# Kernel tuning notes

Measured on AMD Instinct MI355X. Metric: run time of the kernel, lower is better.

Reference implementation:

```python
import jax, jax.numpy as jnp
import numpy as np

LORA_SCALING = 1.0 / 4.0  # lora_alpha / lora_rank
NUM_HEADS = 16
HEAD_DIM = 64
ROPE_BASE = 20000.0


def rotate_half(x):
    x1, x2 = jnp.split(x, 2, axis=-1)
    return jnp.concatenate([-x2, x1], axis=-1)


def setup_inputs() -> dict:
    key = jax.random.key(0)
    ks = jax.random.split(key, 8)
    B, S, D = 8, 1024, 1024
    hidden_states = jax.random.normal(ks[0], (B, S, D), jnp.float32)
    attention_mask = jnp.zeros((B, 1, 1, S), jnp.float32)
    # real rotary tables (HF style: duplicated half-dim freqs)
    inv_freq = 1.0 / (ROPE_BASE ** (jnp.arange(0, HEAD_DIM, 2, dtype=jnp.float32) / HEAD_DIM))
    t = jnp.arange(S, dtype=jnp.float32)
    freqs = jnp.outer(t, inv_freq)                      # [S, hd/2]
    emb = jnp.concatenate([freqs, freqs], axis=-1)      # [S, hd]
    cos = jnp.broadcast_to(jnp.cos(emb)[None], (B, S, HEAD_DIM))
    sin = jnp.broadcast_to(jnp.sin(emb)[None], (B, S, HEAD_DIM))
    adapter_mask = jax.random.randint(ks[1], (B,), 0, 5, jnp.int32)
    Wqkv_weight = jax.random.normal(ks[2], (3 * D, D), jnp.float32) * 0.02
    Wqkv_bias = jax.random.normal(ks[3], (3 * D,), jnp.float32) * 0.02
    lora_A = jax.random.normal(ks[4], (5, 4, D), jnp.float32) * 0.02
    lora_B = jax.random.normal(ks[5], (5, 3 * D, 4), jnp.float32) * 0.02
    return dict(hidden_states=hidden_states, attention_mask=attention_mask,
                cos=cos, sin=sin, adapter_mask=adapter_mask,
                Wqkv_weight=Wqkv_weight, Wqkv_bias=Wqkv_bias,
                lora_A=lora_A, lora_B=lora_B)


def reference(hidden_states, attention_mask, cos, sin, adapter_mask,
              Wqkv_weight, Wqkv_bias, lora_A, lora_B):
    B, S, D = hidden_states.shape
    H, hd = NUM_HEADS, HEAD_DIM
    # fused QKV projection with per-task LoRA (gather adapters per batch row)
    base = jnp.einsum('bsd,od->bso', hidden_states, Wqkv_weight) + Wqkv_bias
    A_t = lora_A[adapter_mask]                    # [B, r, D]
    B_t = lora_B[adapter_mask]                    # [B, 3D, r]
    lo = jnp.einsum('bsd,brd->bsr', hidden_states, A_t)
    delta = jnp.einsum('bsr,bor->bso', lo, B_t) * LORA_SCALING
    qkv = (base + delta).reshape(B, S, 3, H, hd)
    q = qkv[:, :, 0].transpose(0, 2, 1, 3)        # [B,H,S,hd]
    k = qkv[:, :, 1].transpose(0, 2, 1, 3)
    v = qkv[:, :, 2].transpose(0, 2, 1, 3)
    # inline RoPE
    c = cos[:, None, :, :]
    s = sin[:, None, :, :]
    q = q * c + rotate_half(q) * s
    k = k * c + rotate_half(k) * s
    # eager SDPA
    scaling = hd ** -0.5
    scores = jnp.einsum('bhqd,bhkd->bhqk', q, k) * scaling + attention_mask
    attn = jax.nn.softmax(scores, axis=-1)
    out = jnp.einsum('bhqk,bhkd->bhqd', attn, v)
    return out.transpose(0, 2, 1, 3).reshape(B, S, H * hd)
```

## Files before the change

kernel.cpp:

```cpp
#include <hip/hip_runtime.h>
#include <hip/hip_bf16.h>
#include <stdint.h>

typedef __attribute__((ext_vector_type(8))) short short8;
typedef __attribute__((ext_vector_type(4))) float f32x4;
typedef unsigned short ushort_t;

#define MFMA16(a, b, c) __builtin_amdgcn_mfma_f32_16x16x32_bf16((a), (b), (c), 0, 0, 0)
#define EXP2F(x) __builtin_amdgcn_exp2f(x)
#define BAR() __builtin_amdgcn_s_barrier()
#define LGKM0() do { asm volatile("s_waitcnt lgkmcnt(0)" ::: "memory"); \
                     __builtin_amdgcn_sched_barrier(0); } while (0)


__device__ __forceinline__ float bf2f(unsigned short u) {
    union { unsigned int i; float f; } x; x.i = ((unsigned int)u) << 16; return x.f;
}
__device__ __forceinline__ unsigned short f2bf(float f) {
    union { float f; unsigned int i; } x; x.f = f;
    unsigned int i = x.i;
    i = i + 0x7FFFu + ((i >> 16) & 1u);
    return (unsigned short)(i >> 16);
}
__device__ __forceinline__ unsigned int pack2(float a, float b) {
    return (unsigned int)f2bf(a) | ((unsigned int)f2bf(b) << 16);
}
__device__ __forceinline__ void glds16(const void* gsrc, void* ldst) {
    __builtin_amdgcn_global_load_lds(
        (const __attribute__((address_space(1))) unsigned int*)gsrc,
        (__attribute__((address_space(3))) unsigned int*)ldst, 16, 0, 0);
}

__global__ __launch_bounds__(64) void prep_kernel(
    const float* __restrict__ hidden,
    const float* __restrict__ W,
    const float* __restrict__ loraA,
    const int* __restrict__ adapter_mask,
    ushort_t* __restrict__ Hb,
    ushort_t* __restrict__ Wb,
    float4* __restrict__ lo)
{
    int blk = blockIdx.x;
    int lane = threadIdx.x;
    if (blk < 8192) {
        int b = blk >> 10;
        int a = adapter_mask[b];
        const float* hp = hidden + (size_t)blk * 1024 + lane * 16;
        float hv[16];
        for (int j = 0; j < 16; ++j) hv[j] = hp[j];
        uint4 p0, p1;
        p0.x = pack2(hv[0], hv[1]);  p0.y = pack2(hv[2], hv[3]);
        p0.z = pack2(hv[4], hv[5]);  p0.w = pack2(hv[6], hv[7]);
        p1.x = pack2(hv[8], hv[9]);  p1.y = pack2(hv[10], hv[11]);
        p1.z = pack2(hv[12], hv[13]); p1.w = pack2(hv[14], hv[15]);
        uint4* hd = (uint4*)(Hb + (size_t)blk * 1024 + lane * 16);
        hd[0] = p0; hd[1] = p1;
        const float* Ap = loraA + (size_t)a * 4096 + lane * 16;
        float acc[4];
        for (int r = 0; r < 4; ++r) {
            const float* ap = Ap + r * 1024;
            float s = 0.f;
            for (int j = 0; j < 16; ++j) s += hv[j] * ap[j];
            acc[r] = s;
        }
        for (int off = 32; off > 0; off >>= 1)
            for (int r = 0; r < 4; ++r) acc[r] += __shfl_xor(acc[r], off);
        if (lane == 0) lo[blk] = make_float4(acc[0], acc[1], acc[2], acc[3]);
    } else {
        int row = blk - 8192;
        const float* wp = W + (size_t)row * 1024 + lane * 16;
        float wv[16];
        for (int j = 0; j < 16; ++j) wv[j] = wp[j];
        uint4 p0, p1;
        p0.x = pack2(wv[0], wv[1]);  p0.y = pack2(wv[2], wv[3]);
        p0.z = pack2(wv[4], wv[5]);  p0.w = pack2(wv[6], wv[7]);
        p1.x = pack2(wv[8], wv[9]);  p1.y = pack2(wv[10], wv[11]);
        p1.z = pack2(wv[12], wv[13]); p1.w = pack2(wv[14], wv[15]);
        uint4* wd = (uint4*)(Wb + (size_t)row * 1024 + lane * 16);
        wd[0] = p0; wd[1] = p1;
    }
}

__global__ __launch_bounds__(512, 2) void qkv_gemm_kernel(
    const ushort_t* __restrict__ Hb,
    const ushort_t* __restrict__ Wb,
    const float* __restrict__ bias,
    const float4* __restrict__ lo,
    const float* __restrict__ loraB,
    const int* __restrict__ adapter_mask,
    const float* __restrict__ cosp,
    const float* __restrict__ sinp,
    ushort_t* __restrict__ qw,
    ushort_t* __restrict__ kw,
    ushort_t* __restrict__ vt)
{
    __shared__ __align__(16) ushort_t As[2][16384];
    __shared__ __align__(16) ushort_t Bs[2][16384];
    int tid = threadIdx.x;
    int wave = tid >> 6, lane = tid & 63, quad = lane >> 4, l16 = lane & 15;
    int wm = wave >> 2, wn = wave & 3;

    int wg = (blockIdx.x & 7) * 48 + (blockIdx.x >> 3);
    int bx = wg % 12, by = wg / 12;
    int n0 = bx * 256;
    int m0 = by * 256;

    int r_ = tid >> 3, c_ = (tid & 7) ^ (r_ & 7);
    const ushort_t* pA0 = Hb + (size_t)(m0 +   0 + r_) * 1024 + c_ * 8;
    const ushort_t* pA1 = Hb + (size_t)(m0 +  64 + r_) * 1024 + c_ * 8;
    const ushort_t* pA2 = Hb + (size_t)(m0 + 128 + r_) * 1024 + c_ * 8;
    const ushort_t* pA3 = Hb + (size_t)(m0 + 192 + r_) * 1024 + c_ * 8;
    const ushort_t* pB0 = Wb + (size_t)(n0 +   0 + r_) * 1024 + c_ * 8;
    const ushort_t* pB1 = Wb + (size_t)(n0 +  64 + r_) * 1024 + c_ * 8;
    const ushort_t* pB2 = Wb + (size_t)(n0 + 128 + r_) * 1024 + c_ * 8;
    const ushort_t* pB3 = Wb + (size_t)(n0 + 192 + r_) * 1024 + c_ * 8;
    char* stA0 = (char*)&As[0][0] + wave * 1024;
    char* stB0 = (char*)&Bs[0][0] + wave * 1024;

    f32x4 acc[8][4];
#pragma unroll
    for (int i = 0; i < 8; ++i)
#pragma unroll
        for (int j = 0; j < 4; ++j) acc[i][j] = (f32x4)0.f;

    glds16(pB0, stB0);          glds16(pB1, stB0 + 8192);
    glds16(pB2, stB0 + 16384);  glds16(pB3, stB0 + 24576);
    glds16(pA0, stA0);          glds16(pA1, stA0 + 8192);
    glds16(pA2, stA0 + 16384);  glds16(pA3, stA0 + 24576);
    glds16(pB0 + 64, stB0 + 32768);          glds16(pB1 + 64, stB0 + 32768 + 8192);
    glds16(pB2 + 64, stB0 + 32768 + 16384);  glds16(pB3 + 64, stB0 + 32768 + 24576);

    short8 bfr[4][2];
    short8 af0[2], af1[2];

#define AREADS(p) do {                                                              \
        int rl0 = (p) * 32 + l16;                                                   \
        int rl1 = rl0 + 16;                                                         \
        int u0 = wm * 2 + (rl0 >> 6), u1 = wm * 2 + (rl1 >> 6);                     \
        int rr0 = rl0 & 63, rr1 = rl1 & 63;                                         \
        af0[0] = *(const short8*)(rdA + u0 * 8192 + (rr0 * 8 + ((quad    ) ^ (rr0 & 7))) * 16); \
        af0[1] = *(const short8*)(rdA + u0 * 8192 + (rr0 * 8 + ((quad + 4) ^ (rr0 & 7))) * 16); \
        af1[0] = *(const short8*)(rdA + u1 * 8192 + (rr1 * 8 + ((quad    ) ^ (rr1 & 7))) * 16); \
        af1[1] = *(const short8*)(rdA + u1 * 8192 + (rr1 * 8 + ((quad + 4) ^ (rr1 & 7))) * 16); \
    } while (0)

#define PMFMA(p) do {                                                    \
        __builtin_amdgcn_s_setprio(1);                                   \
        acc[2*(p)  ][0] = MFMA16(af0[0], bfr[0][0], acc[2*(p)  ][0]);    \
        acc[2*(p)  ][1] = MFMA16(af0[0], bfr[1][0], acc[2*(p)  ][1]);    \
        acc[2*(p)  ][2] = MFMA16(af0[0], bfr[2][0], acc[2*(p)  ][2]);    \
        acc[2*(p)  ][3] = MFMA16(af0[0], bfr[3][0], acc[2*(p)  ][3]);    \
        acc[2*(p)+1][0] = MFMA16(af1[0], bfr[0][0], acc[2*(p)+1][0]);    \
        acc[2*(p)+1][1] = MFMA16(af1[0], bfr[1][0], acc[2*(p)+1][1]);    \
        acc[2*(p)+1][2] = MFMA16(af1[0], bfr[2][0], acc[2*(p)+1][2]);    \
        acc[2*(p)+1][3] = MFMA16(af1[0], bfr[3][0], acc[2*(p)+1][3]);    \
        acc[2*(p)  ][0] = MFMA16(af0[1], bfr[0][1], acc[2*(p)  ][0]);    \
        acc[2*(p)  ][1] = MFMA16(af0[1], bfr[1][1], acc[2*(p)  ][1]);    \
        acc[2*(p)  ][2] = MFMA16(af0[1], bfr[2][1], acc[2*(p)  ][2]);    \
        acc[2*(p)  ][3] = MFMA16(af0[1], bfr[3][1], acc[2*(p)  ][3]);    \
        acc[2*(p)+1][0] = MFMA16(af1[1], bfr[0][1], acc[2*(p)+1][0]);    \
        acc[2*(p)+1][1] = MFMA16(af1[1], bfr[1][1], acc[2*(p)+1][1]);    \
        acc[2*(p)+1][2] = MFMA16(af1[1], bfr[2][1], acc[2*(p)+1][2]);    \
        acc[2*(p)+1][3] = MFMA16(af1[1], bfr[3][1], acc[2*(p)+1][3]);    \
        __builtin_amdgcn_s_setprio(0);                                   \
    } while (0)

#pragma unroll 2
    for (int t = 0; t < 16; ++t) {
        int cur = t & 1;
        const char* rdA = (const char*)&As[0][0] + cur * 32768;
        const char* rdB = (const char*)&Bs[0][0] + cur * 32768;
        char* sA = stA0 + (cur ^ 1) * 32768;
        char* sB = stB0 + cur * 32768;
        int kA = (t + 1) << 6;
        int kB = (t + 2) << 6;
        bool doA = (t < 15), doB = (t < 14);

        if (t < 15) { asm volatile("s_waitcnt vmcnt(4)" ::: "memory"); }
        else        { asm volatile("s_waitcnt vmcnt(0)" ::: "memory"); }
        BAR();
#pragma unroll
        for (int ni = 0; ni < 4; ++ni) {
            int rb = ni * 16 + l16;
            bfr[ni][0] = *(const short8*)(rdB + wn * 8192 + (rb * 8 + ((quad    ) ^ (rb & 7))) * 16);
            bfr[ni][1] = *(const short8*)(rdB + wn * 8192 + (rb * 8 + ((quad + 4) ^ (rb & 7))) * 16);
        }
        AREADS(0);
        if (doA) { glds16(pA0 + kA, sA); glds16(pA1 + kA, sA + 8192); }
        BAR();
        LGKM0();
        PMFMA(0);

        BAR();
        AREADS(1);
        if (doA) { glds16(pA2 + kA, sA + 16384); glds16(pA3 + kA, sA + 24576); }
        BAR();
        LGKM0();
        PMFMA(1);

        BAR();
        AREADS(2);
        if (doB) { glds16(pB0 + kB, sB); glds16(pB1 + kB, sB + 8192); }
        BAR();
        LGKM0();
        PMFMA(2);

        BAR();
        AREADS(3);
        if (doB) { glds16(pB2 + kB, sB + 16384); glds16(pB3 + kB, sB + 24576); }
        BAR();
        LGKM0();
        PMFMA(3);
    }
#undef AREADS
#undef PMFMA

    int t_qkv = n0 >> 10;
    int b = m0 >> 10;
    int a_idx = adapter_mask[b];
    float bi[4], bb[4][4];
    int cpos[4], chh[4];
#pragma unroll
    for (int ni = 0; ni < 4; ++ni) {
        int c = n0 + wn * 64 + ni * 16 + l16;
        bi[ni] = bias[c];
        const float* Bp = loraB + ((size_t)a_idx * 3072 + c) * 4;
        bb[ni][0] = Bp[0]; bb[ni][1] = Bp[1]; bb[ni][2] = Bp[2]; bb[ni][3] = Bp[3];
        cpos[ni] = c & 63; chh[ni] = (c >> 6) & 15;
    }
#pragma unroll
    for (int mi = 0; mi < 8; ++mi) {
        float vals[4][4];
        int mrow0 = m0 + wm * 128 + mi * 16 + quad * 4;
#pragma unroll
        for (int r = 0; r < 4; ++r) {
            float4 lov = lo[mrow0 + r];
#pragma unroll
            for (int ni = 0; ni < 4; ++ni)
                vals[r][ni] = acc[mi][ni][r] + bi[ni]
                      + 0.25f * (lov.x * bb[ni][0] + lov.y * bb[ni][1]
                               + lov.z * bb[ni][2] + lov.w * bb[ni][3]);
        }
        int s0 = mrow0 & 1023;
        if (t_qkv < 2) {
#pragma unroll
            for (int r = 0; r < 4; ++r) {
                int s = s0 + r;
                size_t cb = ((size_t)b * 1024 + s) * 64;
                float cA = cosp[cb + l16],      sA_ = sinp[cb + l16];
                float cB = cosp[cb + 16 + l16], sB_ = sinp[cb + 16 + l16];
                float w0 = vals[r][0] * cA - vals[r][2] * sA_;
                float w2 = vals[r][2] * cA + vals[r][0] * sA_;
                float w1 = vals[r][1] * cB - vals[r][3] * sB_;
                float w3 = vals[r][3] * cB + vals[r][1] * sB_;
                float v[4] = {w0, w1, w2, w3};
#pragma unroll
                for (int ni = 0; ni < 4; ++ni) {
                    size_t bh = (size_t)b * 16 + chh[ni];
                    ushort_t ob = f2bf(v[ni]);
                    if (t_qkv == 0) qw[(bh * 1024 + s) * 64 + cpos[ni]] = ob;
                    else            kw[(bh * 1024 + s) * 64 + cpos[ni]] = ob;
                }
            }
        } else {
#pragma unroll
            for (int ni = 0; ni < 4; ++ni) {
                uint2 pk;
                pk.x = pack2(vals[0][ni], vals[1][ni]);
                pk.y = pack2(vals[2][ni], vals[3][ni]);
                size_t bh = (size_t)b * 16 + chh[ni];
                *(uint2*)&vt[(bh * 64 + cpos[ni]) * 1024 + s0] = pk;
            }
        }
    }
}

__global__ __launch_bounds__(256) void attn_kernel(
    const ushort_t* __restrict__ qw,
    const ushort_t* __restrict__ kw,
    const ushort_t* __restrict__ vt,
    const float* __restrict__ mask,
    float* __restrict__ out)
{
    __shared__ __align__(16) ushort_t Kt[3][4096];
    __shared__ __align__(16) ushort_t Vt[3][4096];
    __shared__ __align__(16) ushort_t Ps[4][32][72];
    __shared__ float mlds[1024];
    const float KSCALE = 0.125f * 1.44269504f;
    int tid = threadIdx.x;
    int wave = tid >> 6, lane = tid & 63, quad = lane >> 4, l16 = lane & 15;
    int id = blockIdx.x;
    int qt = id >> 7;
    int bh = id & 127;
    int b = bh >> 4, h = bh & 15;
    size_t base = (size_t)bh * 65536;
    int q0 = qt * 128 + wave * 32;

    for (int i = tid; i < 1024; i += 256) mlds[i] = mask[b * 1024 + i] * 1.44269504f;

    const ushort_t* kbase = kw + base;
    const ushort_t* vbase = vt + base;

    int n0 = tid, n1 = tid + 256;
    int r0 = n0 >> 3, c0 = (n0 & 7) ^ (r0 & 7);
    int r1 = n1 >> 3, c1 = (n1 & 7) ^ (r1 & 7);

    short8 qf[2][2];
    for (int mt = 0; mt < 2; ++mt)
        for (int kt = 0; kt < 2; ++kt)
            qf[mt][kt] = *(const short8*)(qw + base + (size_t)(q0 + mt * 16 + l16) * 64 + kt * 32 + quad * 8);

    f32x4 oacc[2][4], sum_acc[2];
    for (int mt = 0; mt < 2; ++mt) {
        sum_acc[mt] = (f32x4)0.f;
        for (int nt = 0; nt < 4; ++nt) oacc[mt][nt] = (f32x4)0.f;
    }

    short8 ones;
    for (int j = 0; j < 8; ++j) ones[j] = (short)0x3F80;

    __syncthreads();

    int koff[4][2], voff[4][2];
    for (int nt = 0; nt < 4; ++nt)
        for (int kt = 0; kt < 2; ++kt) {
            int rr = nt * 16 + l16;
            int cc = (kt * 4 + quad) ^ (rr & 7);
            koff[nt][kt] = (rr * 8 + cc) * 8;
            voff[nt][kt] = (rr * 8 + cc) * 8;
        }

    {
        char* kd = (char*)&Kt[0][0] + wave * 1024;
        char* vd = (char*)&Vt[0][0] + wave * 1024;
        glds16(kbase + (size_t)r0 * 64 + c0 * 8, kd);
        glds16(kbase + (size_t)r1 * 64 + c1 * 8, kd + 4096);
        glds16(vbase + (size_t)r0 * 1024 + c0 * 8, vd);
        glds16(vbase + (size_t)r1 * 1024 + c1 * 8, vd + 4096);
        kd = (char*)&Kt[1][0] + wave * 1024;
        vd = (char*)&Vt[1][0] + wave * 1024;
        glds16(kbase + (size_t)(64 + r0) * 64 + c0 * 8, kd);
        glds16(kbase + (size_t)(64 + r1) * 64 + c1 * 8, kd + 4096);
        glds16(vbase + (size_t)r0 * 1024 + 64 + c0 * 8, vd);
        glds16(vbase + (size_t)r1 * 1024 + 64 + c1 * 8, vd + 4096);
    }

    const ushort_t* kR  = &Kt[0][0];  const ushort_t* vR  = &Vt[0][0];
    const ushort_t* kN1 = &Kt[1][0];  const ushort_t* vN1 = &Vt[1][0];
    const ushort_t* kN2 = &Kt[2][0];  const ushort_t* vN2 = &Vt[2][0];

    for (int it = 0; it < 16; ++it) {
        int kt0 = it * 64;
        if (it < 15) { asm volatile("s_waitcnt vmcnt(4)" ::: "memory"); }
        else         { asm volatile("s_waitcnt vmcnt(0)" ::: "memory"); }
        BAR();
        __builtin_amdgcn_sched_barrier(0);
        if (it < 14) {
            int kn = kt0 + 128;
            char* kd = (char*)kN2 + wave * 1024;
            char* vd = (char*)vN2 + wave * 1024;
            glds16(kbase + (size_t)(kn + r0) * 64 + c0 * 8, kd);
            glds16(kbase + (size_t)(kn + r1) * 64 + c1 * 8, kd + 4096);
            glds16(vbase + (size_t)r0 * 1024 + kn + c0 * 8, vd);
            glds16(vbase + (size_t)r1 * 1024 + kn + c1 * 8, vd + 4096);
        }
        short8 kf[4][2];
        for (int nt = 0; nt < 4; ++nt)
            for (int kt = 0; kt < 2; ++kt)
                kf[nt][kt] = *(const short8*)&kR[koff[nt][kt]];
        f32x4 sacc[2][4];
        for (int mt = 0; mt < 2; ++mt)
            for (int nt = 0; nt < 4; ++nt) {
                f32x4 z = (f32x4)0.f;
                z = MFMA16(qf[mt][0], kf[nt][0], z);
                z = MFMA16(qf[mt][1], kf[nt][1], z);
                sacc[mt][nt] = z;
            }
        float mv[4];
        for (int nt = 0; nt < 4; ++nt) mv[nt] = mlds[kt0 + nt * 16 + l16];
        for (int mt = 0; mt < 2; ++mt)
            for (int nt = 0; nt < 4; ++nt)
                for (int r = 0; r < 4; ++r) {
                    float p = EXP2F(sacc[mt][nt][r] * KSCALE + mv[nt]);
                    Ps[wave][mt * 16 + quad * 4 + r][nt * 16 + l16] = f2bf(p);
                }
        short8 pf[2][2];
        for (int mt = 0; mt < 2; ++mt)
            for (int kt = 0; kt < 2; ++kt)
                pf[mt][kt] = *(const short8*)&Ps[wave][mt * 16 + l16][kt * 32 + quad * 8];
        short8 vf[4][2];
        for (int nt = 0; nt < 4; ++nt)
            for (int kt = 0; kt < 2; ++kt)
                vf[nt][kt] = *(const short8*)&vR[voff[nt][kt]];
        for (int mt = 0; mt < 2; ++mt) {
            for (int nt = 0; nt < 4; ++nt) {
                oacc[mt][nt] = MFMA16(pf[mt][0], vf[nt][0], oacc[mt][nt]);
                oacc[mt][nt] = MFMA16(pf[mt][1], vf[nt][1], oacc[mt][nt]);
            }
            sum_acc[mt] = MFMA16(pf[mt][0], ones, sum_acc[mt]);
            sum_acc[mt] = MFMA16(pf[mt][1], ones, sum_acc[mt]);
        }
        const ushort_t* tk = kR; kR = kN1; kN1 = kN2; kN2 = tk;
        const ushort_t* tv = vR; vR = vN1; vN1 = vN2; vN2 = tv;
    }

    for (int mt = 0; mt < 2; ++mt) {
        for (int r = 0; r < 4; ++r) {
            float inv = 1.f / sum_acc[mt][r];
            int s = q0 + mt * 16 + quad * 4 + r;
            size_t ob = ((size_t)b * 1024 + s) * 1024 + h * 64;
            for (int nt = 0; nt < 4; ++nt)
                out[ob + nt * 16 + l16] = oacc[mt][nt][r] * inv;
        }
    }
}

extern "C" void kernel_launch(void* const* d_in, const int* in_sizes, int n_in,
                              void* d_out, int out_size, void* d_ws, size_t ws_size,
                              hipStream_t stream)
{
    const float* hidden = (const float*)d_in[0];
    const float* mask   = (const float*)d_in[1];
    const float* cosp   = (const float*)d_in[2];
    const float* sinp   = (const float*)d_in[3];
    const int* adapter_mask = (const int*)d_in[4];
    const float* W      = (const float*)d_in[5];
    const float* bias   = (const float*)d_in[6];
    const float* loraA  = (const float*)d_in[7];
    const float* loraB  = (const float*)d_in[8];
    float* out = (float*)d_out;

    char* ws = (char*)d_ws;
    float4* lo = (float4*)ws;
    ushort_t* qw = (ushort_t*)(ws + (1 << 20));
    ushort_t* kw = qw + (size_t)8 * 16 * 1024 * 64;
    ushort_t* vt = kw + (size_t)8 * 16 * 1024 * 64;

    ushort_t* Hb = (ushort_t*)d_out;
    ushort_t* Wb = Hb + (size_t)8192 * 1024;

    prep_kernel<<<11264, 64, 0, stream>>>(hidden, W, loraA, adapter_mask, Hb, Wb, lo);
    qkv_gemm_kernel<<<384, 512, 0, stream>>>(Hb, Wb, bias, lo, loraB, adapter_mask,
                                             cosp, sinp, qw, kw, vt);
    attn_kernel<<<1024, 256, 0, stream>>>(qw, kw, vt, mask, out);
}
```

Baseline: 249.6 us.

## Collapse four-phase GEMM main loop into a two-barrier schedule

Replaces the QKV GEMM inner loop. It used four sub-phases per K-step, each with two barriers, explicit lgkmcnt waits and sched barriers. The new loop has two barriers per K-step: all A prefetches are issued at the top, the B fragments are read and waited on once, then the B prefetches are issued. The A fragment LDS reads are left inside an unrolled MFMA loop for the compiler to schedule. The goal is lower barrier and wait overhead, at the cost of losing the hand-tuned interleaving of LDS reads, global-to-LDS loads and MFMAs.

```diff
diff --git a/kernel.cpp b/kernel.cpp
--- a/kernel.cpp
+++ b/kernel.cpp
@@ -9,8 +9,6 @@
 #define MFMA16(a, b, c) __builtin_amdgcn_mfma_f32_16x16x32_bf16((a), (b), (c), 0, 0, 0)
 #define EXP2F(x) __builtin_amdgcn_exp2f(x)
 #define BAR() __builtin_amdgcn_s_barrier()
-#define LGKM0() do { asm volatile("s_waitcnt lgkmcnt(0)" ::: "memory"); \
-                     __builtin_amdgcn_sched_barrier(0); } while (0)
 
 
 __device__ __forceinline__ float bf2f(unsigned short u) {
@@ -130,41 +128,6 @@
     glds16(pB0 + 64, stB0 + 32768);          glds16(pB1 + 64, stB0 + 32768 + 8192);
     glds16(pB2 + 64, stB0 + 32768 + 16384);  glds16(pB3 + 64, stB0 + 32768 + 24576);
 
-    short8 bfr[4][2];
-    short8 af0[2], af1[2];
-
-#define AREADS(p) do {                                                              \
-        int rl0 = (p) * 32 + l16;                                                   \
-        int rl1 = rl0 + 16;                                                         \
-        int u0 = wm * 2 + (rl0 >> 6), u1 = wm * 2 + (rl1 >> 6);                     \
-        int rr0 = rl0 & 63, rr1 = rl1 & 63;                                         \
-        af0[0] = *(const short8*)(rdA + u0 * 8192 + (rr0 * 8 + ((quad    ) ^ (rr0 & 7))) * 16); \
-        af0[1] = *(const short8*)(rdA + u0 * 8192 + (rr0 * 8 + ((quad + 4) ^ (rr0 & 7))) * 16); \
-        af1[0] = *(const short8*)(rdA + u1 * 8192 + (rr1 * 8 + ((quad    ) ^ (rr1 & 7))) * 16); \
-        af1[1] = *(const short8*)(rdA + u1 * 8192 + (rr1 * 8 + ((quad + 4) ^ (rr1 & 7))) * 16); \
-    } while (0)
-
-#define PMFMA(p) do {                                                    \
-        __builtin_amdgcn_s_setprio(1);                                   \
-        acc[2*(p)  ][0] = MFMA16(af0[0], bfr[0][0], acc[2*(p)  ][0]);    \
-        acc[2*(p)  ][1] = MFMA16(af0[0], bfr[1][0], acc[2*(p)  ][1]);    \
-        acc[2*(p)  ][2] = MFMA16(af0[0], bfr[2][0], acc[2*(p)  ][2]);    \
-        acc[2*(p)  ][3] = MFMA16(af0[0], bfr[3][0], acc[2*(p)  ][3]);    \
-        acc[2*(p)+1][0] = MFMA16(af1[0], bfr[0][0], acc[2*(p)+1][0]);    \
-        acc[2*(p)+1][1] = MFMA16(af1[0], bfr[1][0], acc[2*(p)+1][1]);    \
-        acc[2*(p)+1][2] = MFMA16(af1[0], bfr[2][0], acc[2*(p)+1][2]);    \
-        acc[2*(p)+1][3] = MFMA16(af1[0], bfr[3][0], acc[2*(p)+1][3]);    \
-        acc[2*(p)  ][0] = MFMA16(af0[1], bfr[0][1], acc[2*(p)  ][0]);    \
-        acc[2*(p)  ][1] = MFMA16(af0[1], bfr[1][1], acc[2*(p)  ][1]);    \
-        acc[2*(p)  ][2] = MFMA16(af0[1], bfr[2][1], acc[2*(p)  ][2]);    \
-        acc[2*(p)  ][3] = MFMA16(af0[1], bfr[3][1], acc[2*(p)  ][3]);    \
-        acc[2*(p)+1][0] = MFMA16(af1[1], bfr[0][1], acc[2*(p)+1][0]);    \
-        acc[2*(p)+1][1] = MFMA16(af1[1], bfr[1][1], acc[2*(p)+1][1]);    \
-        acc[2*(p)+1][2] = MFMA16(af1[1], bfr[2][1], acc[2*(p)+1][2]);    \
-        acc[2*(p)+1][3] = MFMA16(af1[1], bfr[3][1], acc[2*(p)+1][3]);    \
-        __builtin_amdgcn_s_setprio(0);                                   \
-    } while (0)
-
 #pragma unroll 2
     for (int t = 0; t < 16; ++t) {
         int cur = t & 1;
@@ -174,46 +137,45 @@
         char* sB = stB0 + cur * 32768;
         int kA = (t + 1) << 6;
         int kB = (t + 2) << 6;
-        bool doA = (t < 15), doB = (t < 14);
 
         if (t < 15) { asm volatile("s_waitcnt vmcnt(4)" ::: "memory"); }
         else        { asm volatile("s_waitcnt vmcnt(0)" ::: "memory"); }
         BAR();
+        if (t < 15) {
+            glds16(pA0 + kA, sA);          glds16(pA1 + kA, sA + 8192);
+            glds16(pA2 + kA, sA + 16384);  glds16(pA3 + kA, sA + 24576);
+        }
+        short8 bfr[4][2];
 #pragma unroll
         for (int ni = 0; ni < 4; ++ni) {
             int rb = ni * 16 + l16;
             bfr[ni][0] = *(const short8*)(rdB + wn * 8192 + (rb * 8 + ((quad    ) ^ (rb & 7))) * 16);
             bfr[ni][1] = *(const short8*)(rdB + wn * 8192 + (rb * 8 + ((quad + 4) ^ (rb & 7))) * 16);
         }
-        AREADS(0);
-        if (doA) { glds16(pA0 + kA, sA); glds16(pA1 + kA, sA + 8192); }
+        asm volatile("s_waitcnt lgkmcnt(0)" ::: "memory");
         BAR();
-        LGKM0();
-        PMFMA(0);
-
-        BAR();
-        AREADS(1);
-        if (doA) { glds16(pA2 + kA, sA + 16384); glds16(pA3 + kA, sA + 24576); }
-        BAR();
-        LGKM0();
-        PMFMA(1);
-
-        BAR();
-        AREADS(2);
-        if (doB) { glds16(pB0 + kB, sB); glds16(pB1 + kB, sB + 8192); }
-        BAR();
-        LGKM0();
-        PMFMA(2);
-
-        BAR();
-        AREADS(3);
-        if (doB) { glds16(pB2 + kB, sB + 16384); glds16(pB3 + kB, sB + 24576); }
-        BAR();
-        LGKM0();
-        PMFMA(3);
-    }
-#undef AREADS
-#undef PMFMA
+        if (t < 14) {
+            glds16(pB0 + kB, sB);          glds16(pB1 + kB, sB + 8192);
+            glds16(pB2 + kB, sB + 16384);  glds16(pB3 + kB, sB + 24576);
+        }
+        __builtin_amdgcn_s_setprio(1);
+#pragma unroll
+        for (int mi = 0; mi < 8; ++mi) {
+            int u = wm * 2 + (mi >> 2);
+            int rr = (mi & 3) * 16 + l16;
+            short8 a0 = *(const short8*)(rdA + u * 8192 + (rr * 8 + ((quad    ) ^ (rr & 7))) * 16);
+            short8 a1 = *(const short8*)(rdA + u * 8192 + (rr * 8 + ((quad + 4) ^ (rr & 7))) * 16);
+            acc[mi][0] = MFMA16(a0, bfr[0][0], acc[mi][0]);
+            acc[mi][1] = MFMA16(a0, bfr[1][0], acc[mi][1]);
+            acc[mi][2] = MFMA16(a0, bfr[2][0], acc[mi][2]);
+            acc[mi][3] = MFMA16(a0, bfr[3][0], acc[mi][3]);
+            acc[mi][0] = MFMA16(a1, bfr[0][1], acc[mi][0]);
+            acc[mi][1] = MFMA16(a1, bfr[1][1], acc[mi][1]);
+            acc[mi][2] = MFMA16(a1, bfr[2][1], acc[mi][2]);
+            acc[mi][3] = MFMA16(a1, bfr[3][1], acc[mi][3]);
+        }
+        __builtin_amdgcn_s_setprio(0);
+    }
 
     int t_qkv = n0 >> 10;
     int b = m0 >> 10;
```

New measurement: 251.0 us. Within noise of the previous version (+0.6%).
